# Kernel optimization log

Measured on AMD Instinct MI355X. Metric: run time of the kernel, lower is better.

## Reference

```python
import jax, jax.numpy as jnp
import numpy as np

B, S, DIN, DOUT = 4, 2048, 4096, 4096

def setup_inputs() -> dict:
    key = jax.random.key(0)
    k1, k2, k3 = jax.random.split(key, 3)
    inp = jax.random.normal(k1, (B, S, DIN), dtype=jnp.float16)
    # int8 quantized weights in [-127, 127]
    qweight = jax.random.randint(k2, (DOUT, DIN), -127, 128, dtype=jnp.int32).astype(jnp.int8)
    # per-output-channel scales, small positive
    qscales = (jax.random.uniform(k3, (DOUT, 1), dtype=jnp.float32) * 0.01 + 1e-4).astype(jnp.float16)
    return {"inp": inp, "qweight": qweight, "qscales": qscales}

def reference(inp, qweight, qscales):
    # Dequantize: int8 * fp16 scale -> fp16 weight [out, in] (matches torch promotion + .to(fp16))
    w = (qweight.astype(jnp.float16) * qscales).astype(jnp.float16)
    # F.linear(inp, w) = inp @ w.T ; note: bias is NOT added in the original forward
    return jnp.einsum("bsd,od->bso", inp, w)
```

## Files before the change

### kernel.cpp

```cpp
#include <hip/hip_runtime.h>
#include <stdint.h>


#define M_DIM 8192
#define N_DIM 4096
#define K_DIM 4096
#define BM 256
#define BN 256
#define BK 32
#define NKT (K_DIM / BK)

typedef _Float16 f16;
typedef f16 f16x8 __attribute__((ext_vector_type(8)));
typedef f16 f16x2 __attribute__((ext_vector_type(2)));
typedef float f32x4 __attribute__((ext_vector_type(4)));

static __device__ __forceinline__ f16x2 cvt2(float a, float b) {
  return __builtin_bit_cast(f16x2, __builtin_amdgcn_cvt_pkrtz(a, b));
}


__global__ __launch_bounds__(256) void conv_a_kernel(
    const float* __restrict__ A, f16* __restrict__ Af)
{
  const size_t stride = (size_t)gridDim.x * blockDim.x;
  size_t i = (size_t)blockIdx.x * blockDim.x + threadIdx.x;
  const size_t n8 = (size_t)M_DIM * K_DIM / 8;
  for (; i < n8; i += stride) {
    const f32x4* p = (const f32x4*)(A + i * 8);
    f32x4 v0 = p[0], v1 = p[1];
    f16x2 a = cvt2(v0.x, v0.y), b = cvt2(v0.z, v0.w);
    f16x2 c = cvt2(v1.x, v1.y), d = cvt2(v1.z, v1.w);
    *(f16x8*)(Af + i * 8) = (f16x8){a.x, a.y, b.x, b.y, c.x, c.y, d.x, d.y};
  }
}

__global__ __launch_bounds__(256) void conv_b2_kernel(
    const int* __restrict__ Qw, const float* __restrict__ Sc,
    f16* __restrict__ Wf2)
{
  const int c16 = blockIdx.x;
  const int t  = threadIdx.x;
  const int l  = t & 63;
  const int g  = t >> 6;
  const int fr = l & 15;
  const int qk = l >> 4;
  const int o  = c16 * 16 + fr;
  const float s = Sc[o];
  const int* qrow = Qw + (size_t)o * K_DIM + qk * 8;
  f16* wbase = Wf2 + (size_t)c16 * 128 * 64 * 8 + (size_t)l * 8;
  for (int kt = g; kt < NKT; kt += 4) {
    const int* q = qrow + kt * 32;
    int4 u0 = *(const int4*)(q);
    int4 u1 = *(const int4*)(q + 4);
    f16x2 a = cvt2((float)u0.x * s, (float)u0.y * s);
    f16x2 b = cvt2((float)u0.z * s, (float)u0.w * s);
    f16x2 c = cvt2((float)u1.x * s, (float)u1.y * s);
    f16x2 d = cvt2((float)u1.z * s, (float)u1.w * s);
    *(f16x8*)(wbase + (size_t)kt * 512) =
        (f16x8){a.x, a.y, b.x, b.y, c.x, c.y, d.x, d.y};
  }
}


#define BARX() __builtin_amdgcn_s_barrier()
#define SCHED0() __builtin_amdgcn_sched_barrier(0)
#define LGKM(n) do { asm volatile("s_waitcnt lgkmcnt(" #n ")" ::: "memory"); \
                     __builtin_amdgcn_sched_barrier(0); } while (0)
#define VMW(n)  do { asm volatile("s_waitcnt vmcnt(" #n ")" ::: "memory"); \
                     __builtin_amdgcn_sched_barrier(0); } while (0)

#define STAGE_A(bi, ktn) do { \
  _Pragma("unroll") \
  for (int _i = 0; _i < 2; ++_i) { \
    const f16* _g = aSrc + (size_t)((st_R + 64 * _i) * 2 + st_h) * K_DIM \
                    + (ktn) * BK + st_s * 8; \
    char* _l = (char*)&As[bi][0] + _i * 8192 + wid * 1024; \
    __builtin_amdgcn_global_load_lds( \
        (const __attribute__((address_space(1))) void*)_g, \
        (__attribute__((address_space(3))) void*)_l, 16, 0, 0); \
  } } while (0)

#define A_LDS(CB, j) (const f16x8*)((const char*)&As[CB][0] + aoff + 2048 * (j))

#define LOAD_B(dst, ktn) do { \
  dst[0] = *(const f16x8*)(bbase + 0 * 524288 + (size_t)(ktn) * 1024); \
  dst[1] = *(const f16x8*)(bbase + 1 * 524288 + (size_t)(ktn) * 1024); \
  dst[2] = *(const f16x8*)(bbase + 2 * 524288 + (size_t)(ktn) * 1024); \
  dst[3] = *(const f16x8*)(bbase + 3 * 524288 + (size_t)(ktn) * 1024); \
  } while (0)

#define MFMA4(mb, B_) do { \
  _Pragma("unroll") \
  for (int _m = 0; _m < 4; ++_m) \
    _Pragma("unroll") \
    for (int _n = 0; _n < 4; ++_n) \
      acc[(mb) + _m][_n] = __builtin_amdgcn_mfma_f32_16x16x32_f16( \
          af[(mb) + _m], B_[_n], acc[(mb) + _m][_n], 0, 0, 0); \
  } while (0)

#define TILE(KT, CUR, NXT, BCUR, BNXT, M1) do { \
  if (M1) { \
    STAGE_A(NXT, (KT) + 1); \
    LOAD_B(BNXT, (KT) + 1); \
  } \
  af[0] = *A_LDS(CUR, 0); af[1] = *A_LDS(CUR, 1); \
  af[2] = *A_LDS(CUR, 2); af[3] = *A_LDS(CUR, 3); \
  af[4] = *A_LDS(CUR, 4); af[5] = *A_LDS(CUR, 5); \
  af[6] = *A_LDS(CUR, 6); af[7] = *A_LDS(CUR, 7); \
  LGKM(4); \
  MFMA4(0, BCUR); \
  LGKM(0); \
  MFMA4(4, BCUR); \
  if (M1) { VMW(4); } else { VMW(0); } \
  BARX(); \
} while (0)

__global__ __launch_bounds__(512, 1) void w8a16_gemm_f16_kernel(
    const f16* __restrict__ Af,
    const f16* __restrict__ Wf2,
    float* __restrict__ Out)
{
  __shared__ __align__(16) f16 As[2][BM * BK];

  const int t    = threadIdx.x;
  const int lane = t & 63;
  const int wid  = t >> 6;
  const int wm   = wid >> 2;
  const int wn   = wid & 3;
  const int fr   = lane & 15;
  const int qk   = lane >> 4;

  const int st_R = t >> 3;
  const int st_x = (t & 7) ^ (st_R & 7);
  const int st_h = st_x >> 2;
  const int st_s = st_x & 3;

  const int ca   = wm * 16 + fr;
  const int aoff = (ca >> 1) * 128
                 + (((((ca & 1) << 2) | qk) ^ ((ca >> 1) & 7)) << 4);

  const int bid = blockIdx.x;
  const int swz = (bid & 7) * 64 + (bid >> 3);
  const int tn  = swz >> 5;
  const int tm  = swz & 31;

  const f16* aSrc = Af + (size_t)tm * BM * K_DIM;

  const char* bbase = (const char*)Wf2
      + ((size_t)(tn * 16 + wn) * 128) * 1024 + (size_t)lane * 16;

  f32x4 acc[8][4] = {};
  f16x8 af[8], bA[4], bB[4];

  STAGE_A(0, 0);
  LOAD_B(bA, 0);
  VMW(4);
  BARX();
  SCHED0();

  for (int kt = 0; kt < NKT - 2; kt += 2) {
    TILE(kt,     0, 1, bA, bB, 1);
    TILE(kt + 1, 1, 0, bB, bA, 1);
  }
  TILE(NKT - 2, 0, 1, bA, bB, 1);
  TILE(NKT - 1, 1, 0, bB, bA, 0);

  const int fq = lane >> 4;
  #pragma unroll
  for (int mi = 0; mi < 8; ++mi) {
    const size_t row = (size_t)tm * BM + (2 * mi + wm) * 16 + fq * 4;
    #pragma unroll
    for (int ni = 0; ni < 4; ++ni) {
      const size_t col = (size_t)tn * BN + ni * 64 + wn * 16 + fr;
      #pragma unroll
      for (int r = 0; r < 4; ++r)
        Out[(row + r) * N_DIM + col] = acc[mi][ni][r];
    }
  }
}


__global__ __launch_bounds__(256) void w8a16_gemm_fb_kernel(
    const float* __restrict__ A, const int* __restrict__ Qw,
    const float* __restrict__ Sc, float* __restrict__ Out)
{
  __shared__ __align__(16) float Asf[2][128 * 32];
  __shared__ __align__(16) f16 Bsf[2][128][32];

  const int t = threadIdx.x, lane = t & 63, wid = t >> 6;
  const int wr = wid >> 1, wc = wid & 1;
  const int nwg = gridDim.x, cpx = nwg >> 3, bid = blockIdx.x;
  const int swz = (bid & 7) * cpx + (bid >> 3);
  const int tn = swz & 31, tm = swz >> 5;
  const size_t a_base = (size_t)tm * 128 * K_DIM;
  const size_t b_base = (size_t)tn * 128 * K_DIM;
  f32x4 acc[4][4] = {};
  const int a_r = t >> 3;
  const int a_slog = (t & 7) ^ ((t >> 3) & 7);

  auto stageA = [&](int buf, int kt) {
    #pragma unroll
    for (int c = 0; c < 4; ++c) {
      const float* g = A + a_base + (size_t)(c * 32 + a_r) * K_DIM + kt * 32 + a_slog * 4;
      char* l = (char*)&Asf[buf][0] + c * 4096 + wid * 1024;
      __builtin_amdgcn_global_load_lds(
          (const __attribute__((address_space(1))) void*)g,
          (__attribute__((address_space(3))) void*)l, 16, 0, 0);
    }
  };
  const int b_r = t >> 3, b_col = (t & 7) * 4;
  auto loadB = [&](int kt, int4* v) {
    #pragma unroll
    for (int c = 0; c < 4; ++c)
      v[c] = *(const int4*)(Qw + b_base + (size_t)(c * 32 + b_r) * K_DIM + kt * 32 + b_col);
  };
  auto writeB = [&](int buf, const int4* v) {
    #pragma unroll
    for (int c = 0; c < 4; ++c) {
      f16x2 lo = cvt2((float)v[c].x, (float)v[c].y);
      f16x2 hi = cvt2((float)v[c].z, (float)v[c].w);
      *(f16x2*)&Bsf[buf][c * 32 + b_r][b_col] = lo;
      *(f16x2*)&Bsf[buf][c * 32 + b_r][b_col + 2] = hi;
    }
  };
  auto compute = [&](int buf) {
    const int fr2 = lane & 15, q = lane >> 4;
    f16x8 af2[4], bf2[4];
    #pragma unroll
    for (int i = 0; i < 4; ++i) {
      const int r = wr * 64 + i * 16 + fr2;
      const float* base = &Asf[buf][0] + r * 32;
      const int s0 = q * 2;
      f32x4 a0 = *(const f32x4*)(base + ((s0 ^ (r & 7)) * 4));
      f32x4 a1 = *(const f32x4*)(base + (((s0 + 1) ^ (r & 7)) * 4));
      f16x2 p0 = cvt2(a0.x, a0.y), p1 = cvt2(a0.z, a0.w);
      f16x2 p2 = cvt2(a1.x, a1.y), p3 = cvt2(a1.z, a1.w);
      af2[i] = (f16x8){p0.x, p0.y, p1.x, p1.y, p2.x, p2.y, p3.x, p3.y};
      bf2[i] = *(const f16x8*)&Bsf[buf][wc * 64 + i * 16 + fr2][q * 8];
    }
    #pragma unroll
    for (int mi = 0; mi < 4; ++mi)
      #pragma unroll
      for (int ni = 0; ni < 4; ++ni)
        acc[mi][ni] = __builtin_amdgcn_mfma_f32_16x16x32_f16(
            af2[mi], bf2[ni], acc[mi][ni], 0, 0, 0);
  };

  { int4 b0[4]; stageA(0, 0); loadB(0, b0); writeB(0, b0); }
  __syncthreads();
  for (int kt = 0; kt < K_DIM / 32; ++kt) {
    const int buf = kt & 1;
    const bool more = (kt + 1) < K_DIM / 32;
    int4 nb[4];
    if (more) { stageA(buf ^ 1, kt + 1); loadB(kt + 1, nb); }
    compute(buf);
    if (more) writeB(buf ^ 1, nb);
    __syncthreads();
  }
  const int fr2 = lane & 15, fq = lane >> 4;
  const int cb = tn * 128 + wc * 64 + fr2;
  const int rb = tm * 128 + wr * 64 + fq * 4;
  #pragma unroll
  for (int ni = 0; ni < 4; ++ni) {
    const float s = Sc[cb + ni * 16];
    #pragma unroll
    for (int mi = 0; mi < 4; ++mi)
      #pragma unroll
      for (int r = 0; r < 4; ++r)
        Out[(size_t)(rb + mi * 16 + r) * N_DIM + (cb + ni * 16)] =
            acc[mi][ni][r] * s;
  }
}

extern "C" void kernel_launch(void* const* d_in, const int* in_sizes, int n_in,
                              void* d_out, int out_size, void* d_ws, size_t ws_size,
                              hipStream_t stream) {
  const float* A  = (const float*)d_in[0];
  const int*   Qw = (const int*)d_in[1];
  const float* Sc = (const float*)d_in[2];
  float*       Out = (float*)d_out;

  const size_t a_bytes = (size_t)M_DIM * K_DIM * sizeof(f16);
  const size_t w_bytes = (size_t)N_DIM * K_DIM * sizeof(f16);

  if (ws_size >= a_bytes + w_bytes) {
    f16* Af  = (f16*)d_ws;
    f16* Wf2 = (f16*)((char*)d_ws + a_bytes);
    conv_a_kernel<<<2048, 256, 0, stream>>>(A, Af);
    conv_b2_kernel<<<N_DIM / 16, 256, 0, stream>>>(Qw, Sc, Wf2);
    dim3 grid((M_DIM / BM) * (N_DIM / BN));
    w8a16_gemm_f16_kernel<<<grid, 512, 0, stream>>>(Af, Wf2, Out);
  } else {
    dim3 grid((M_DIM / 128) * (N_DIM / 128));
    w8a16_gemm_fb_kernel<<<grid, 256, 0, stream>>>(A, Qw, Sc, Out);
  }
}
```

Measured before the change: 352.9 us.

## Pre-swizzle activations into MFMA fragment layout and drop LDS staging

```diff
diff --git a/kernel.cpp b/kernel.cpp
--- a/kernel.cpp
+++ b/kernel.cpp
@@ -20,18 +20,26 @@
 }
 
 
-__global__ __launch_bounds__(256) void conv_a_kernel(
-    const float* __restrict__ A, f16* __restrict__ Af)
-{
-  const size_t stride = (size_t)gridDim.x * blockDim.x;
-  size_t i = (size_t)blockIdx.x * blockDim.x + threadIdx.x;
-  const size_t n8 = (size_t)M_DIM * K_DIM / 8;
-  for (; i < n8; i += stride) {
-    const f32x4* p = (const f32x4*)(A + i * 8);
-    f32x4 v0 = p[0], v1 = p[1];
+__global__ __launch_bounds__(256) void conv_a2_kernel(
+    const float* __restrict__ A, f16* __restrict__ Af2)
+{
+  const int m16 = blockIdx.x;
+  const int t  = threadIdx.x;
+  const int l  = t & 63;
+  const int g  = t >> 6;
+  const int fr = l & 15;
+  const int qk = l >> 4;
+  const int o  = m16 * 16 + fr;
+  const float* arow = A + (size_t)o * K_DIM + qk * 8;
+  f16* wbase = Af2 + (size_t)m16 * 128 * 64 * 8 + (size_t)l * 8;
+  for (int kt = g; kt < NKT; kt += 4) {
+    const float* p = arow + kt * 32;
+    f32x4 v0 = *(const f32x4*)(p);
+    f32x4 v1 = *(const f32x4*)(p + 4);
     f16x2 a = cvt2(v0.x, v0.y), b = cvt2(v0.z, v0.w);
     f16x2 c = cvt2(v1.x, v1.y), d = cvt2(v1.z, v1.w);
-    *(f16x8*)(Af + i * 8) = (f16x8){a.x, a.y, b.x, b.y, c.x, c.y, d.x, d.y};
+    *(f16x8*)(wbase + (size_t)kt * 512) =
+        (f16x8){a.x, a.y, b.x, b.y, c.x, c.y, d.x, d.y};
   }
 }
 
@@ -63,25 +71,16 @@
 }
 
 
-#define BARX() __builtin_amdgcn_s_barrier()
-#define SCHED0() __builtin_amdgcn_sched_barrier(0)
-#define LGKM(n) do { asm volatile("s_waitcnt lgkmcnt(" #n ")" ::: "memory"); \
-                     __builtin_amdgcn_sched_barrier(0); } while (0)
-#define VMW(n)  do { asm volatile("s_waitcnt vmcnt(" #n ")" ::: "memory"); \
-                     __builtin_amdgcn_sched_barrier(0); } while (0)
-
-#define STAGE_A(bi, ktn) do { \
-  _Pragma("unroll") \
-  for (int _i = 0; _i < 2; ++_i) { \
-    const f16* _g = aSrc + (size_t)((st_R + 64 * _i) * 2 + st_h) * K_DIM \
-                    + (ktn) * BK + st_s * 8; \
-    char* _l = (char*)&As[bi][0] + _i * 8192 + wid * 1024; \
-    __builtin_amdgcn_global_load_lds( \
-        (const __attribute__((address_space(1))) void*)_g, \
-        (__attribute__((address_space(3))) void*)_l, 16, 0, 0); \
-  } } while (0)
-
-#define A_LDS(CB, j) (const f16x8*)((const char*)&As[CB][0] + aoff + 2048 * (j))
+#define LOAD_A(dst, ktn) do { \
+  dst[0] = *(const f16x8*)(abase + 0 * 262144 + (size_t)(ktn) * 1024); \
+  dst[1] = *(const f16x8*)(abase + 1 * 262144 + (size_t)(ktn) * 1024); \
+  dst[2] = *(const f16x8*)(abase + 2 * 262144 + (size_t)(ktn) * 1024); \
+  dst[3] = *(const f16x8*)(abase + 3 * 262144 + (size_t)(ktn) * 1024); \
+  dst[4] = *(const f16x8*)(abase + 4 * 262144 + (size_t)(ktn) * 1024); \
+  dst[5] = *(const f16x8*)(abase + 5 * 262144 + (size_t)(ktn) * 1024); \
+  dst[6] = *(const f16x8*)(abase + 6 * 262144 + (size_t)(ktn) * 1024); \
+  dst[7] = *(const f16x8*)(abase + 7 * 262144 + (size_t)(ktn) * 1024); \
+  } while (0)
 
 #define LOAD_B(dst, ktn) do { \
   dst[0] = *(const f16x8*)(bbase + 0 * 524288 + (size_t)(ktn) * 1024); \
@@ -90,81 +89,50 @@
   dst[3] = *(const f16x8*)(bbase + 3 * 524288 + (size_t)(ktn) * 1024); \
   } while (0)
 
-#define MFMA4(mb, B_) do { \
+#define TILE(KT, AC, BC, AN, BN_, M1) do { \
+  if (M1) { LOAD_A(AN, (KT) + 1); LOAD_B(BN_, (KT) + 1); } \
   _Pragma("unroll") \
-  for (int _m = 0; _m < 4; ++_m) \
+  for (int _m = 0; _m < 8; ++_m) \
     _Pragma("unroll") \
     for (int _n = 0; _n < 4; ++_n) \
-      acc[(mb) + _m][_n] = __builtin_amdgcn_mfma_f32_16x16x32_f16( \
-          af[(mb) + _m], B_[_n], acc[(mb) + _m][_n], 0, 0, 0); \
+      acc[_m][_n] = __builtin_amdgcn_mfma_f32_16x16x32_f16( \
+          AC[_m], BC[_n], acc[_m][_n], 0, 0, 0); \
   } while (0)
 
-#define TILE(KT, CUR, NXT, BCUR, BNXT, M1) do { \
-  if (M1) { \
-    STAGE_A(NXT, (KT) + 1); \
-    LOAD_B(BNXT, (KT) + 1); \
-  } \
-  af[0] = *A_LDS(CUR, 0); af[1] = *A_LDS(CUR, 1); \
-  af[2] = *A_LDS(CUR, 2); af[3] = *A_LDS(CUR, 3); \
-  af[4] = *A_LDS(CUR, 4); af[5] = *A_LDS(CUR, 5); \
-  af[6] = *A_LDS(CUR, 6); af[7] = *A_LDS(CUR, 7); \
-  LGKM(4); \
-  MFMA4(0, BCUR); \
-  LGKM(0); \
-  MFMA4(4, BCUR); \
-  if (M1) { VMW(4); } else { VMW(0); } \
-  BARX(); \
-} while (0)
-
 __global__ __launch_bounds__(512, 1) void w8a16_gemm_f16_kernel(
-    const f16* __restrict__ Af,
+    const f16* __restrict__ Af2,
     const f16* __restrict__ Wf2,
     float* __restrict__ Out)
 {
-  __shared__ __align__(16) f16 As[2][BM * BK];
-
   const int t    = threadIdx.x;
   const int lane = t & 63;
   const int wid  = t >> 6;
   const int wm   = wid >> 2;
   const int wn   = wid & 3;
   const int fr   = lane & 15;
-  const int qk   = lane >> 4;
-
-  const int st_R = t >> 3;
-  const int st_x = (t & 7) ^ (st_R & 7);
-  const int st_h = st_x >> 2;
-  const int st_s = st_x & 3;
-
-  const int ca   = wm * 16 + fr;
-  const int aoff = (ca >> 1) * 128
-                 + (((((ca & 1) << 2) | qk) ^ ((ca >> 1) & 7)) << 4);
 
   const int bid = blockIdx.x;
   const int swz = (bid & 7) * 64 + (bid >> 3);
   const int tn  = swz >> 5;
   const int tm  = swz & 31;
 
-  const f16* aSrc = Af + (size_t)tm * BM * K_DIM;
-
+  const char* abase = (const char*)Af2
+      + ((size_t)(tm * 16 + wm) * 128) * 1024 + (size_t)lane * 16;
   const char* bbase = (const char*)Wf2
       + ((size_t)(tn * 16 + wn) * 128) * 1024 + (size_t)lane * 16;
 
   f32x4 acc[8][4] = {};
-  f16x8 af[8], bA[4], bB[4];
-
-  STAGE_A(0, 0);
+  f16x8 aA[8], aB[8], bA[4], bB[4];
+
+  LOAD_A(aA, 0);
   LOAD_B(bA, 0);
-  VMW(4);
-  BARX();
-  SCHED0();
 
   for (int kt = 0; kt < NKT - 2; kt += 2) {
-    TILE(kt,     0, 1, bA, bB, 1);
-    TILE(kt + 1, 1, 0, bB, bA, 1);
-  }
-  TILE(NKT - 2, 0, 1, bA, bB, 1);
-  TILE(NKT - 1, 1, 0, bB, bA, 0);
+    TILE(kt,     aA, bA, aB, bB, 1);
+    TILE(kt + 1, aB, bB, aA, bA, 1);
+  }
+  TILE(NKT - 2, aA, bA, aB, bB, 1);
+  TILE(NKT - 1, aB, bB, aA, bA, 0);
 
   const int fq = lane >> 4;
   #pragma unroll
@@ -285,12 +253,12 @@
   const size_t w_bytes = (size_t)N_DIM * K_DIM * sizeof(f16);
 
   if (ws_size >= a_bytes + w_bytes) {
-    f16* Af  = (f16*)d_ws;
+    f16* Af2 = (f16*)d_ws;
     f16* Wf2 = (f16*)((char*)d_ws + a_bytes);
-    conv_a_kernel<<<2048, 256, 0, stream>>>(A, Af);
+    conv_a2_kernel<<<M_DIM / 16, 256, 0, stream>>>(A, Af2);
     conv_b2_kernel<<<N_DIM / 16, 256, 0, stream>>>(Qw, Sc, Wf2);
     dim3 grid((M_DIM / BM) * (N_DIM / BN));
-    w8a16_gemm_f16_kernel<<<grid, 512, 0, stream>>>(Af, Wf2, Out);
+    w8a16_gemm_f16_kernel<<<grid, 512, 0, stream>>>(Af2, Wf2, Out);
   } else {
     dim3 grid((M_DIM / 128) * (N_DIM / 128));
     w8a16_gemm_fb_kernel<<<grid, 256, 0, stream>>>(A, Qw, Sc, Out);
```

Result: slower. 445.6 us (+26.3%).
